# Kernel tuning notes

Hardware: AMD Instinct MI355X
Metric: run time of the kernel (lower is better)

The kernel has to match this reference:

```python
import jax, jax.numpy as jnp
import numpy as np

EMBED_DIM = 1024
NUM_HEADS = 16
HEAD_DIM = EMBED_DIM // NUM_HEADS
SCALE = HEAD_DIM ** -0.5
BATCH, SEQ = 4, 2048


def setup_inputs() -> dict:
    key = jax.random.key(0)
    ks = jax.random.split(key, 9)
    s = EMBED_DIM ** -0.5
    return {
        "query": jax.random.normal(ks[0], (BATCH, SEQ, EMBED_DIM), jnp.float32),
        "Wq": jax.random.normal(ks[1], (EMBED_DIM, EMBED_DIM), jnp.float32) * s,
        "bq": jax.random.normal(ks[2], (EMBED_DIM,), jnp.float32) * 0.02,
        "Wk": jax.random.normal(ks[3], (EMBED_DIM, EMBED_DIM), jnp.float32) * s,
        "bk": jax.random.normal(ks[4], (EMBED_DIM,), jnp.float32) * 0.02,
        "Wv": jax.random.normal(ks[5], (EMBED_DIM, EMBED_DIM), jnp.float32) * s,
        "bv": jax.random.normal(ks[6], (EMBED_DIM,), jnp.float32) * 0.02,
        "Wo": jax.random.normal(ks[7], (EMBED_DIM, EMBED_DIM), jnp.float32) * s,
        "bo": jax.random.normal(ks[8], (EMBED_DIM,), jnp.float32) * 0.02,
    }


def reference(query, Wq, bq, Wk, bk, Wv, bv, Wo, bo):
    B, T, E = query.shape
    H, D = NUM_HEADS, HEAD_DIM
    # projections (torch Linear: x @ W.T + b); key=value=query (self-attention)
    q = (query @ Wq.T + bq).reshape(B, T, H, D).transpose(0, 2, 1, 3)  # [B,H,T,D]
    k = (query @ Wk.T + bk).reshape(B, T, H, D).transpose(0, 2, 1, 3)
    v = (query @ Wv.T + bv).reshape(B, T, H, D).transpose(0, 2, 1, 3)
    scores = jnp.einsum("bhtd,bhsd->bhts", q, k) * SCALE  # [B,H,T,T]
    probs = jax.nn.softmax(scores, axis=-1)
    ctx = jnp.einsum("bhts,bhsd->bhtd", probs, v)  # [B,H,T,D]
    ctx = ctx.transpose(0, 2, 1, 3).reshape(B, T, E)
    out = ctx @ Wo.T + bo
    return out
```

## Files before the change

kernel.cpp:

```cpp
#include <hip/hip_runtime.h>
#include <cstdint>

#define DEV __device__ __forceinline__

using short8   = __attribute__((ext_vector_type(8))) short;
using floatx4  = __attribute__((ext_vector_type(4))) float;
using ushortx4 = __attribute__((ext_vector_type(4))) unsigned short;
using intx4    = __attribute__((ext_vector_type(4))) int;

#define MFMA_BF16(a, b, c) __builtin_amdgcn_mfma_f32_16x16x32_bf16((a), (b), (c), 0, 0, 0)

static constexpr float QK_SCALE_LOG2E = 0.18033688011112042f;

DEV unsigned short f2bf(float f) {
  unsigned int u = __builtin_bit_cast(unsigned int, f);
  u += 0x7FFFu + ((u >> 16) & 1u);
  return (unsigned short)(u >> 16);
}

DEV int cvt_pk_bf16(float lo, float hi) {
  int r;
  asm("v_cvt_pk_bf16_f32 %0, %1, %2" : "=v"(r) : "v"(lo), "v"(hi));
  return r;
}

DEV void gload_lds16(const void* g, void* l) {
  __builtin_amdgcn_global_load_lds(
      (const __attribute__((address_space(1))) void*)g,
      (__attribute__((address_space(3))) void*)l, 16, 0, 0);
}

__global__ void cvt_f32_bf16(const float* __restrict__ src,
                             unsigned short* __restrict__ dst, int n4) {
  int i = blockIdx.x * blockDim.x + threadIdx.x;
  if (i >= n4) return;
  float4 v = reinterpret_cast<const float4*>(src)[i];
  ushortx4 o = {f2bf(v.x), f2bf(v.y), f2bf(v.z), f2bf(v.w)};
  reinterpret_cast<ushortx4*>(dst)[i] = o;
}

__global__ void cvt_w4(const float* __restrict__ w0, const float* __restrict__ w1,
                       const float* __restrict__ w2, const float* __restrict__ w3,
                       unsigned short* __restrict__ dst) {
  int i = blockIdx.x * blockDim.x + threadIdx.x;
  int b = i >> 18;
  const float* src = (b == 0) ? w0 : (b == 1) ? w1 : (b == 2) ? w2 : w3;
  int off = i & 0x3FFFF;
  float4 v = reinterpret_cast<const float4*>(src)[off];
  ushortx4 o = {f2bf(v.x), f2bf(v.y), f2bf(v.z), f2bf(v.w)};
  reinterpret_cast<ushortx4*>(dst)[i] = o;
}

DEV void stage128x64(const unsigned short* gbase, int ld, unsigned short* lds, int tid) {
#pragma unroll
  for (int j = 0; j < 4; ++j) {
    int s = j * 256 + tid;
    int row = s >> 3, slot = s & 7;
    int chunk = slot ^ (row & 7);
    gload_lds16(gbase + row * ld + chunk * 8, (char*)lds + s * 16);
  }
}

template <int KMODE>
DEV void stage64x64(const unsigned short* gbase, int ld, unsigned short* lds, int tid) {
#pragma unroll
  for (int j = 0; j < 2; ++j) {
    int s = j * 256 + tid;
    int row = s >> 3, slot = s & 7;
    int mask = KMODE ? ((row & 3) | ((row >> 1) & 4)) : (row & 7);
    int chunk = slot ^ mask;
    gload_lds16(gbase + row * ld + chunk * 8, (char*)lds + s * 16);
  }
}

__global__ __launch_bounds__(256, 2) void gemm_qkv(
    const unsigned short* __restrict__ A,
    const unsigned short* __restrict__ Wqkv,
    const float* __restrict__ bq, const float* __restrict__ bk,
    const float* __restrict__ bv,
    unsigned short* __restrict__ Qb, unsigned short* __restrict__ Kb,
    unsigned short* __restrict__ Vtb) {
  __shared__ __attribute__((aligned(16))) unsigned short As[128 * 64];
  __shared__ __attribute__((aligned(16))) unsigned short Bs[128 * 64];
  const int tid = threadIdx.x;
  const int wv = tid >> 6, lane = tid & 63;
  const int g = lane >> 4, rc = lane & 15;
  const int wr = wv >> 1, wc = wv & 1;
  const int nt = blockIdx.x >> 3;
  const int n0 = (blockIdx.x & 7) * 128;
  const int m0 = blockIdx.y * 128;
  const float* bias = (nt == 0) ? bq : (nt == 1) ? bk : bv;

  floatx4 acc[4][4] = {};
  const unsigned short* Ag = A + (size_t)m0 * 1024;
  const unsigned short* Wg = Wqkv + ((size_t)nt << 20) + (size_t)n0 * 1024;

  for (int kt = 0; kt < 16; ++kt) {
    stage128x64(Ag + kt * 64, 1024, As, tid);
    stage128x64(Wg + kt * 64, 1024, Bs, tid);
    __syncthreads();
    short8 af[4][2], bf[4][2];
#pragma unroll
    for (int m = 0; m < 4; ++m)
#pragma unroll
      for (int kk = 0; kk < 2; ++kk) {
        int row = wr * 64 + m * 16 + rc;
        int slot = (kk * 4 + g) ^ (row & 7);
        af[m][kk] = *reinterpret_cast<const short8*>(As + row * 64 + slot * 8);
      }
#pragma unroll
    for (int n = 0; n < 4; ++n)
#pragma unroll
      for (int kk = 0; kk < 2; ++kk) {
        int row = wc * 64 + n * 16 + rc;
        int slot = (kk * 4 + g) ^ (row & 7);
        bf[n][kk] = *reinterpret_cast<const short8*>(Bs + row * 64 + slot * 8);
      }
#pragma unroll
    for (int m = 0; m < 4; ++m)
#pragma unroll
      for (int n = 0; n < 4; ++n) {
        acc[m][n] = MFMA_BF16(af[m][0], bf[n][0], acc[m][n]);
        acc[m][n] = MFMA_BF16(af[m][1], bf[n][1], acc[m][n]);
      }
    __syncthreads();
  }

#pragma unroll
  for (int m = 0; m < 4; ++m) {
    const int gm = m0 + wr * 64 + m * 16 + g * 4;
#pragma unroll
    for (int n = 0; n < 4; ++n) {
      const int gn = n0 + wc * 64 + n * 16 + rc;
      const float bs = bias[gn];
      floatx4 v = acc[m][n];
      if (nt == 2) {
        const int bb = gm >> 11, t0 = gm & 2047;
        const int hh = gn >> 6, dd = gn & 63;
        ushortx4 p = {f2bf(v[0] + bs), f2bf(v[1] + bs), f2bf(v[2] + bs), f2bf(v[3] + bs)};
        *reinterpret_cast<ushortx4*>(Vtb + ((size_t)((bb * 16 + hh) * 64 + dd)) * 2048 + t0) = p;
      } else {
        unsigned short* O = (nt == 0) ? Qb : Kb;
        const float sc = (nt == 0) ? QK_SCALE_LOG2E : 1.0f;
#pragma unroll
        for (int i = 0; i < 4; ++i)
          O[(size_t)(gm + i) * 1024 + gn] = f2bf((v[i] + bs) * sc);
      }
    }
  }
}

__global__ __launch_bounds__(256, 2) void gemm_out(
    const unsigned short* __restrict__ A,
    const unsigned short* __restrict__ W,
    const float* __restrict__ bias,
    float* __restrict__ out) {
  __shared__ __attribute__((aligned(16))) unsigned short As[128 * 64];
  __shared__ __attribute__((aligned(16))) unsigned short Bs[128 * 64];
  const int tid = threadIdx.x;
  const int wv = tid >> 6, lane = tid & 63;
  const int g = lane >> 4, rc = lane & 15;
  const int wr = wv >> 1, wc = wv & 1;
  const int m0 = blockIdx.y * 128, n0 = blockIdx.x * 128;

  floatx4 acc[4][4] = {};
  const unsigned short* Ag = A + (size_t)m0 * 1024;
  const unsigned short* Wg = W + (size_t)n0 * 1024;

  for (int kt = 0; kt < 16; ++kt) {
    stage128x64(Ag + kt * 64, 1024, As, tid);
    stage128x64(Wg + kt * 64, 1024, Bs, tid);
    __syncthreads();
    short8 af[4][2], bf[4][2];
#pragma unroll
    for (int m = 0; m < 4; ++m)
#pragma unroll
      for (int kk = 0; kk < 2; ++kk) {
        int row = wr * 64 + m * 16 + rc;
        int slot = (kk * 4 + g) ^ (row & 7);
        af[m][kk] = *reinterpret_cast<const short8*>(As + row * 64 + slot * 8);
      }
#pragma unroll
    for (int n = 0; n < 4; ++n)
#pragma unroll
      for (int kk = 0; kk < 2; ++kk) {
        int row = wc * 64 + n * 16 + rc;
        int slot = (kk * 4 + g) ^ (row & 7);
        bf[n][kk] = *reinterpret_cast<const short8*>(Bs + row * 64 + slot * 8);
      }
#pragma unroll
    for (int m = 0; m < 4; ++m)
#pragma unroll
      for (int n = 0; n < 4; ++n) {
        acc[m][n] = MFMA_BF16(af[m][0], bf[n][0], acc[m][n]);
        acc[m][n] = MFMA_BF16(af[m][1], bf[n][1], acc[m][n]);
      }
    __syncthreads();
  }

#pragma unroll
  for (int m = 0; m < 4; ++m) {
    const int gm = m0 + wr * 64 + m * 16 + g * 4;
#pragma unroll
    for (int n = 0; n < 4; ++n) {
      const int gn = n0 + wc * 64 + n * 16 + rc;
      const float bs = bias[gn];
#pragma unroll
      for (int i = 0; i < 4; ++i) out[(size_t)(gm + i) * 1024 + gn] = acc[m][n][i] + bs;
    }
  }
}

__global__ __launch_bounds__(256, 4) void attn_fwd(
    const unsigned short* __restrict__ Q,
    const unsigned short* __restrict__ K,
    const unsigned short* __restrict__ Vt,
    unsigned short* __restrict__ ctx) {
  __shared__ __attribute__((aligned(16))) unsigned short Ks0[64 * 64];
  __shared__ __attribute__((aligned(16))) unsigned short Ks1[64 * 64];
  __shared__ __attribute__((aligned(16))) unsigned short Vs0[64 * 64];
  __shared__ __attribute__((aligned(16))) unsigned short Vs1[64 * 64];
  const int tid = threadIdx.x;
  const int wv = tid >> 6, lane = tid & 63;
  const int g = lane >> 4, rc = lane & 15;
  const int f = blockIdx.x;
  const int i_ = f >> 3;
  const int bh = (f & 7) * 8 + (i_ & 7);
  const int qb = i_ >> 3;
  const int b = bh >> 4, h = bh & 15;
  const int q0 = qb * 128 + wv * 32;

  short8 qfr[2][2];
  {
    const unsigned short* Qg = Q + (size_t)(b * 2048 + q0 + rc) * 1024 + h * 64 + g * 8;
#pragma unroll
    for (int q_ = 0; q_ < 2; ++q_)
#pragma unroll
      for (int kk = 0; kk < 2; ++kk)
        qfr[q_][kk] = *reinterpret_cast<const short8*>(Qg + q_ * 16 * 1024 + kk * 32);
  }

  const unsigned short* Kg = K + (size_t)b * 2048 * 1024 + h * 64;
  const unsigned short* Vg = Vt + (size_t)bh * 64 * 2048;

  const int i4 = rc & 3, g4 = rc >> 2;
  const int kmask = i4 | ((g4 & 1) << 2);
  const int koff0 = ((g4 * 8 + i4) * 64 + ((g)     ^ kmask) * 8) * 2;
  const int koff1 = ((g4 * 8 + i4) * 64 + ((4 + g) ^ kmask) * 8) * 2;
  const int vmask = rc & 7;
  const int voff0 = (rc * 64 + ((g)     ^ vmask) * 8) * 2;
  const int voff1 = (rc * 64 + ((4 + g) ^ vmask) * 8) * 2;

  const int one2 = 0x3F803F80;
  intx4 ones_i = (rc == 0) ? intx4{one2, one2, one2, one2} : intx4{0, 0, 0, 0};
  const short8 vf_ones = __builtin_bit_cast(short8, ones_i);

  floatx4 acc[2][4] = {};
  floatx4 acc5[2] = {};

  auto tile_compute = [&](const unsigned short* KsB, const unsigned short* VsB) {
    floatx4 sv[2][4] = {};
    __builtin_amdgcn_s_setprio(1);
#pragma unroll
    for (int nf = 0; nf < 4; ++nf) {
      const int ro = ((nf >> 1) * 32 + (nf & 1) * 4) * 128;
      short8 kf0 = *reinterpret_cast<const short8*>((const char*)KsB + ro + koff0);
      short8 kf1 = *reinterpret_cast<const short8*>((const char*)KsB + ro + koff1);
      sv[0][nf] = MFMA_BF16(kf0, qfr[0][0], sv[0][nf]);
      sv[0][nf] = MFMA_BF16(kf1, qfr[0][1], sv[0][nf]);
      sv[1][nf] = MFMA_BF16(kf0, qfr[1][0], sv[1][nf]);
      sv[1][nf] = MFMA_BF16(kf1, qfr[1][1], sv[1][nf]);
    }
    __builtin_amdgcn_s_setprio(0);

#pragma unroll
    for (int q_ = 0; q_ < 2; ++q_)
#pragma unroll
      for (int nf = 0; nf < 4; ++nf)
#pragma unroll
        for (int i = 0; i < 4; ++i)
          sv[q_][nf][i] = __builtin_amdgcn_exp2f(sv[q_][nf][i]);

#pragma unroll
    for (int kb = 0; kb < 2; ++kb) {
      intx4 w0, w1;
#pragma unroll
      for (int w = 0; w < 4; ++w) {
        const int nf = 2 * kb + (w >> 1), ii = (w & 1) * 2;
        w0[w] = cvt_pk_bf16(sv[0][nf][ii], sv[0][nf][ii + 1]);
        w1[w] = cvt_pk_bf16(sv[1][nf][ii], sv[1][nf][ii + 1]);
      }
      short8 pb0 = __builtin_bit_cast(short8, w0);
      short8 pb1 = __builtin_bit_cast(short8, w1);
      const int vo = kb ? voff1 : voff0;
      __builtin_amdgcn_s_setprio(1);
#pragma unroll
      for (int nd = 0; nd < 4; ++nd) {
        short8 vf = *reinterpret_cast<const short8*>((const char*)VsB + nd * 2048 + vo);
        acc[0][nd] = MFMA_BF16(vf, pb0, acc[0][nd]);
        acc[1][nd] = MFMA_BF16(vf, pb1, acc[1][nd]);
      }
      acc5[0] = MFMA_BF16(vf_ones, pb0, acc5[0]);
      acc5[1] = MFMA_BF16(vf_ones, pb1, acc5[1]);
      __builtin_amdgcn_s_setprio(0);
    }
  };

  stage64x64<1>(Kg, 1024, Ks0, tid);
  stage64x64<0>(Vg, 2048, Vs0, tid);
  __syncthreads();

  for (int t = 0; t < 32; t += 2) {
    stage64x64<1>(Kg + (size_t)(t + 1) * 64 * 1024, 1024, Ks1, tid);
    stage64x64<0>(Vg + (t + 1) * 64, 2048, Vs1, tid);
    tile_compute(Ks0, Vs0);
    __syncthreads();
    if (t + 2 < 32) {
      stage64x64<1>(Kg + (size_t)(t + 2) * 64 * 1024, 1024, Ks0, tid);
      stage64x64<0>(Vg + (t + 2) * 64, 2048, Vs0, tid);
    }
    tile_compute(Ks1, Vs1);
    __syncthreads();
  }

#pragma unroll
  for (int q_ = 0; q_ < 2; ++q_) {
    const float l = __shfl(acc5[q_][0], rc);
    const float inv = 1.0f / l;
    unsigned short* Cp = ctx + (size_t)(b * 2048 + q0 + q_ * 16 + rc) * 1024 + h * 64 + g * 4;
#pragma unroll
    for (int nd = 0; nd < 4; ++nd) {
      ushortx4 o = {f2bf(acc[q_][nd][0] * inv), f2bf(acc[q_][nd][1] * inv),
                    f2bf(acc[q_][nd][2] * inv), f2bf(acc[q_][nd][3] * inv)};
      *reinterpret_cast<ushortx4*>(Cp + nd * 16) = o;
    }
  }
}

extern "C" void kernel_launch(void* const* d_in, const int* in_sizes, int n_in,
                              void* d_out, int out_size, void* d_ws, size_t ws_size,
                              hipStream_t stream) {
  (void)in_sizes; (void)n_in; (void)out_size; (void)ws_size;
  const float* x  = (const float*)d_in[0];
  const float* Wq = (const float*)d_in[1];
  const float* bq = (const float*)d_in[2];
  const float* Wk = (const float*)d_in[3];
  const float* bk = (const float*)d_in[4];
  const float* Wv = (const float*)d_in[5];
  const float* bv = (const float*)d_in[6];
  const float* Wo = (const float*)d_in[7];
  const float* bo = (const float*)d_in[8];

  unsigned short* Xb  = (unsigned short*)d_ws;
  unsigned short* Wqb = Xb + (size_t)8192 * 1024;
  unsigned short* Wob = Wqb + (size_t)3 * 1024 * 1024;
  unsigned short* Vtb = Wob + (size_t)1024 * 1024;
  unsigned short* Ctx = Xb;
  unsigned short* Qb = (unsigned short*)d_out;
  unsigned short* Kb = Qb + (size_t)8192 * 1024;

  cvt_f32_bf16<<<8192, 256, 0, stream>>>(x, Xb, 8192 * 1024 / 4);
  cvt_w4<<<4096, 256, 0, stream>>>(Wq, Wk, Wv, Wo, Wqb);

  gemm_qkv<<<dim3(24, 64), 256, 0, stream>>>(Xb, Wqb, bq, bk, bv, Qb, Kb, Vtb);
  attn_fwd<<<1024, 256, 0, stream>>>(Qb, Kb, Vtb, Ctx);
  gemm_out<<<dim3(8, 64), 256, 0, stream>>>(Ctx, Wob, bo, (float*)d_out);
}
```

Before: 163.5 us.

## Triple-buffer K/V tiles in attention with vmcnt-gated single barrier

Moves the attention kernel's K/V staging from double to triple buffering in LDS, issuing loads two tiles ahead. Each iteration now waits on the vector-memory counter and uses one barrier instead of two __syncthreads, so global load latency overlaps with more compute. The extra LDS buffers lower the occupancy hint from 4 to 3 blocks per CU. The hardcoded vmcnt(4) assumes the exact number of outstanding loads per stage, which is fragile if the staging code changes.

After: 165.5 us. No clear change (+1.2%).

```diff
diff --git a/kernel.cpp b/kernel.cpp
--- a/kernel.cpp
+++ b/kernel.cpp
@@ -211,15 +211,17 @@
   }
 }
 
-__global__ __launch_bounds__(256, 4) void attn_fwd(
+__global__ __launch_bounds__(256, 3) void attn_fwd(
     const unsigned short* __restrict__ Q,
     const unsigned short* __restrict__ K,
     const unsigned short* __restrict__ Vt,
     unsigned short* __restrict__ ctx) {
   __shared__ __attribute__((aligned(16))) unsigned short Ks0[64 * 64];
   __shared__ __attribute__((aligned(16))) unsigned short Ks1[64 * 64];
+  __shared__ __attribute__((aligned(16))) unsigned short Ks2[64 * 64];
   __shared__ __attribute__((aligned(16))) unsigned short Vs0[64 * 64];
   __shared__ __attribute__((aligned(16))) unsigned short Vs1[64 * 64];
+  __shared__ __attribute__((aligned(16))) unsigned short Vs2[64 * 64];
   const int tid = threadIdx.x;
   const int wv = tid >> 6, lane = tid & 63;
   const int g = lane >> 4, rc = lane & 15;
@@ -306,21 +308,29 @@
     }
   };
 
-  stage64x64<1>(Kg, 1024, Ks0, tid);
-  stage64x64<0>(Vg, 2048, Vs0, tid);
-  __syncthreads();
-
-  for (int t = 0; t < 32; t += 2) {
-    stage64x64<1>(Kg + (size_t)(t + 1) * 64 * 1024, 1024, Ks1, tid);
-    stage64x64<0>(Vg + (t + 1) * 64, 2048, Vs1, tid);
-    tile_compute(Ks0, Vs0);
-    __syncthreads();
+  const unsigned short *K0 = Ks0, *K1 = Ks1, *K2 = Ks2;
+  const unsigned short *V0 = Vs0, *V1 = Vs1, *V2 = Vs2;
+
+  stage64x64<1>(Kg, 1024, (unsigned short*)K0, tid);
+  stage64x64<0>(Vg, 2048, (unsigned short*)V0, tid);
+  stage64x64<1>(Kg + (size_t)64 * 1024, 1024, (unsigned short*)K1, tid);
+  stage64x64<0>(Vg + 64, 2048, (unsigned short*)V1, tid);
+
+  for (int t = 0; t < 32; ++t) {
+    if (t < 31) {
+      asm volatile("s_waitcnt vmcnt(4)" ::: "memory");
+    } else {
+      asm volatile("s_waitcnt vmcnt(0)" ::: "memory");
+    }
+    __builtin_amdgcn_s_barrier();
+    __builtin_amdgcn_sched_barrier(0);
     if (t + 2 < 32) {
-      stage64x64<1>(Kg + (size_t)(t + 2) * 64 * 1024, 1024, Ks0, tid);
-      stage64x64<0>(Vg + (t + 2) * 64, 2048, Vs0, tid);
-    }
-    tile_compute(Ks1, Vs1);
-    __syncthreads();
+      stage64x64<1>(Kg + (size_t)(t + 2) * 64 * 1024, 1024, (unsigned short*)K2, tid);
+      stage64x64<0>(Vg + (t + 2) * 64, 2048, (unsigned short*)V2, tid);
+    }
+    tile_compute(K0, V0);
+    const unsigned short* kt_ = K0; K0 = K1; K1 = K2; K2 = kt_;
+    const unsigned short* vt_ = V0; V0 = V1; V1 = V2; V2 = vt_;
   }
 
 #pragma unroll
```
